# Performance work log

Hardware: AMD Instinct MI355X
Metric: run time of the kernel (lower is better)

Reference implementation:

```python
import jax, jax.numpy as jnp
import numpy as np

N = 100000
E = 3200000
D_IN = 256
D_HID = 256
D_OUT = 128
EPS = 1e-12


def setup_inputs() -> dict:
    key = jax.random.key(0)
    ks = jax.random.split(key, 8)
    x = jax.random.normal(ks[0], (N, D_IN), dtype=jnp.float32)
    edge_src = jax.random.randint(ks[1], (E,), 0, N, dtype=jnp.int32)
    edge_dst = jax.random.randint(ks[2], (E,), 0, N, dtype=jnp.int32)
    # mean aggregation: each row of the sparse adj sums to 1 -> val = 1/deg(src row)
    deg = jax.ops.segment_sum(jnp.ones((E,), jnp.float32), edge_src, num_segments=N)
    edge_val = 1.0 / jnp.maximum(deg, 1.0)[edge_src]
    # Xavier-uniform linear weights (torch Linear: y = x @ W.T + b); store as [in, out]
    def xavier(k, fan_in, fan_out):
        lim = jnp.sqrt(6.0 / (fan_in + fan_out))
        return jax.random.uniform(k, (fan_in, fan_out), jnp.float32, -lim, lim)
    W1 = xavier(ks[3], 2 * D_IN, D_HID)
    b1 = jnp.zeros((D_HID,), jnp.float32)
    W2 = xavier(ks[4], 2 * D_HID, D_OUT)
    b2 = jnp.zeros((D_OUT,), jnp.float32)
    return {"x": x, "edge_src": edge_src, "edge_dst": edge_dst, "edge_val": edge_val,
            "W1": W1, "b1": b1, "W2": W2, "b2": b2}


def _sage_layer(feat, edge_src, edge_dst, edge_val, W, b):
    # spmm: out[i] = sum_j adj[i,j] * feat[j]  (COO rows=edge_src, cols=edge_dst)
    msg = feat[edge_dst] * edge_val[:, None]              # [E, d]
    neigh = jax.ops.segment_sum(msg, edge_src, num_segments=feat.shape[0])  # [N, d]
    combined = jnp.concatenate([feat, neigh], axis=1) @ W + b  # [N, d_out]
    # F.normalize(p=2, dim=1): x / max(||x||_2, eps)
    norm = jnp.sqrt(jnp.sum(combined * combined, axis=1, keepdims=True))
    return combined / jnp.maximum(norm, EPS)


def reference(x, edge_src, edge_dst, edge_val, W1, b1, W2, b2):
    h = _sage_layer(x, edge_src, edge_dst, edge_val, W1, b1)
    h = jax.nn.relu(h)
    # dropout is identity at inference (training=False)
    return _sage_layer(h, edge_src, edge_dst, edge_val, W2, b2)
```

## Files before the change

### kernel.cpp

```cpp
#include <hip/hip_runtime.h>


#define N_NODES 100000
#define N_EDGES 3200000
#define DF      256
#define NRANGE  4

typedef __bf16 bf16x8 __attribute__((ext_vector_type(8)));
typedef float  f32x4  __attribute__((ext_vector_type(4)));
typedef float  f32x2  __attribute__((ext_vector_type(2)));

__device__ __forceinline__ ushort f2bf(float f){
  uint u = __float_as_uint(f);
  u += 0x7fffu + ((u >> 16) & 1u);
  return (ushort)(u >> 16);
}
__device__ __forceinline__ float bflo(uint u){ return __uint_as_float(u << 16); }
__device__ __forceinline__ float bfhi(uint u){ return __uint_as_float(u & 0xffff0000u); }


__global__ void k_cvt(const float4* __restrict__ x4, uint4* __restrict__ outb,
                      uint2* __restrict__ outq, int n8, int* __restrict__ deg, int nz){
  int i = blockIdx.x * blockDim.x + threadIdx.x;
  if(i < nz) deg[i] = 0;
  if(i >= n8) return;
  const float4 p = x4[2*i], q = x4[2*i+1];
  uint4 o;
  o.x = (uint)f2bf(p.x) | ((uint)f2bf(p.y) << 16);
  o.y = (uint)f2bf(p.z) | ((uint)f2bf(p.w) << 16);
  o.z = (uint)f2bf(q.x) | ((uint)f2bf(q.y) << 16);
  o.w = (uint)f2bf(q.z) | ((uint)f2bf(q.w) << 16);
  outb[i] = o;
  uint w0 = __builtin_amdgcn_cvt_pk_fp8_f32(p.x, p.y, 0u, false);
  w0      = __builtin_amdgcn_cvt_pk_fp8_f32(p.z, p.w, w0, true);
  uint w1 = __builtin_amdgcn_cvt_pk_fp8_f32(q.x, q.y, 0u, false);
  w1      = __builtin_amdgcn_cvt_pk_fp8_f32(q.z, q.w, w1, true);
  outq[i] = make_uint2(w0, w1);
}


__global__ void k_deg(const int* __restrict__ esrc, const float* __restrict__ eval,
                      int* __restrict__ deg, int E){
  int i = blockIdx.x * blockDim.x + threadIdx.x;
  if(i < E){
    const int   s = __builtin_nontemporal_load(&esrc[i]);
    const float v = __builtin_nontemporal_load(&eval[i]);
    deg[s] = (int)roundf(1.0f / v);
  }
}


__global__ void k_scan1(const int* __restrict__ deg, int* __restrict__ rowptr,
                        int* __restrict__ partials, int n){
  __shared__ int s[256];
  const int t = threadIdx.x;
  const int base = blockIdx.x * 1024 + t * 4;
  int v[4], run[4];
  #pragma unroll
  for(int j = 0; j < 4; j++) v[j] = (base + j < n) ? deg[base + j] : 0;
  int sum = 0;
  #pragma unroll
  for(int j = 0; j < 4; j++){ run[j] = sum; sum += v[j]; }
  s[t] = sum;
  __syncthreads();
  for(int off = 1; off < 256; off <<= 1){
    int x = (t >= off) ? s[t - off] : 0;
    __syncthreads();
    s[t] += x;
    __syncthreads();
  }
  const int texcl = s[t] - sum;
  #pragma unroll
  for(int j = 0; j < 4; j++) if(base + j < n) rowptr[base + j] = texcl + run[j];
  if(t == 255) partials[blockIdx.x] = s[255];
}

__global__ void k_scan2(int* __restrict__ partials, int nb,
                        int* __restrict__ rowptr, int n, int E){
  __shared__ int s[128];
  const int t = threadIdx.x;
  int v = (t < nb) ? partials[t] : 0;
  s[t] = v;
  __syncthreads();
  for(int off = 1; off < 128; off <<= 1){
    int x = (t >= off) ? s[t - off] : 0;
    __syncthreads();
    s[t] += x;
    __syncthreads();
  }
  if(t < nb) partials[t] = s[t] - v;
  if(t == 0) rowptr[n] = E;
}


__global__ void k_scan3(int* __restrict__ rowptr, const int* __restrict__ partials,
                        int* __restrict__ cursor, int n){
  int i = blockIdx.x * blockDim.x + threadIdx.x;
  if(i < n){
    const int v = rowptr[i] + partials[i >> 10];
    rowptr[i] = v;
    cursor[i] = v;
  }
}


__global__ void k_fill(const int* __restrict__ src, const int* __restrict__ dst,
                       int* __restrict__ cursor, int* __restrict__ col,
                       int E, int lo, int hi){
  int i = blockIdx.x * blockDim.x + threadIdx.x;
  if(i < E){
    const int r = src[i];
    if(r >= lo && r < hi){
      const int p = atomicAdd(&cursor[r], 1);
      col[p] = dst[i];
    }
  }
}


__device__ __forceinline__ void pack_frag(const float* __restrict__ W, uint4* __restrict__ Wp,
                                          int DOUT, int ksteps, int krow0, int tid){
  const int l   = tid & 63;
  const int s   = (tid >> 6) % ksteps;
  const int n   = tid / (64 * ksteps);
  const int grp = l >> 4, li = l & 15;
  const int col = n * 16 + li;
  ushort b[8];
  #pragma unroll
  for(int i = 0; i < 8; i++){
    const int k = krow0 + s * 32 + grp * 8 + i;
    b[i] = f2bf(W[(size_t)k * DOUT + col]);
  }
  uint4 o;
  o.x = (uint)b[0] | ((uint)b[1] << 16);
  o.y = (uint)b[2] | ((uint)b[3] << 16);
  o.z = (uint)b[4] | ((uint)b[5] << 16);
  o.w = (uint)b[6] | ((uint)b[7] << 16);
  Wp[tid] = o;
}

__global__ void k_packall(const float* __restrict__ W1, const float* __restrict__ W2,
                          uint4* __restrict__ Wp1, uint4* __restrict__ Wp2a,
                          uint4* __restrict__ Wp2b){
  const int tid = blockIdx.x * blockDim.x + threadIdx.x;
  if(tid < 16384)       pack_frag(W1, Wp1,  256, 16,   0, tid);
  else if(tid < 20480)  pack_frag(W2, Wp2a, 128,  8,   0, tid - 16384);
  else if(tid < 24576)  pack_frag(W2, Wp2b, 128,  8, 256, tid - 20480);
}


template<int RB>
__global__ __launch_bounds__(256)
void k_gather_q(const uchar* __restrict__ xq, const int* __restrict__ rowptr,
                const int* __restrict__ colidx, ushort* __restrict__ nbuf, int Nn){
  constexpr int LPR = RB / 16;
  constexpr int EPG = 64 / LPR;
  const int node = (blockIdx.x * blockDim.x + threadIdx.x) >> 6;
  const int lane = threadIdx.x & 63;
  if(node >= Nn) return;
  const int half = lane / LPR;
  const int li   = lane % LPR;
  const int s0 = rowptr[node];
  const int s1 = rowptr[node + 1];
  const float invd = (s1 > s0) ? (1.0f / (float)(s1 - s0)) : 0.0f;
  const uint cmax = (uint)(Nn - 1);
  float a[16];
  #pragma unroll
  for(int i = 0; i < 16; i++) a[i] = 0.f;

  #define DECODE_ACC(v)                                                        \
    {                                                                          \
      const uint uu[4] = {(v).x, (v).y, (v).z, (v).w};                         \
      _Pragma("unroll")                                                        \
      for(int m = 0; m < 4; m++){                                              \
        f32x2 lo = __builtin_amdgcn_cvt_pk_f32_fp8(uu[m], false);              \
        f32x2 hi = __builtin_amdgcn_cvt_pk_f32_fp8(uu[m], true);               \
        a[m*4+0] += lo.x; a[m*4+1] += lo.y;                                    \
        a[m*4+2] += hi.x; a[m*4+3] += hi.y;                                    \
      }                                                                        \
    }

  int e = s0;
  for(; e + 4 * EPG <= s1; e += 4 * EPG){
    uint c[4];
    #pragma unroll
    for(int j = 0; j < 4; j++)
      c[j] = min((uint)__builtin_nontemporal_load(&colidx[e + j * EPG + half]), cmax);
    uint4 v[4];
    #pragma unroll
    for(int j = 0; j < 4; j++) v[j] = *(const uint4*)(xq + (size_t)c[j] * RB + li * 16);
    #pragma unroll
    for(int j = 0; j < 4; j++) DECODE_ACC(v[j]);
  }
  for(; e + EPG <= s1; e += EPG){
    const uint c = min((uint)__builtin_nontemporal_load(&colidx[e + half]), cmax);
    const uint4 v = *(const uint4*)(xq + (size_t)c * RB + li * 16);
    DECODE_ACC(v);
  }
  if(half < s1 - e){
    const uint c = min((uint)__builtin_nontemporal_load(&colidx[e + half]), cmax);
    const uint4 v = *(const uint4*)(xq + (size_t)c * RB + li * 16);
    DECODE_ACC(v);
  }
  #undef DECODE_ACC

  #pragma unroll
  for(int off = LPR; off < 64; off <<= 1)
    #pragma unroll
    for(int i = 0; i < 16; i++) a[i] += __shfl_xor(a[i], off);

  if(lane < LPR){
    uint4 o1, o2;
    o1.x = (uint)f2bf(a[ 0]*invd) | ((uint)f2bf(a[ 1]*invd) << 16);
    o1.y = (uint)f2bf(a[ 2]*invd) | ((uint)f2bf(a[ 3]*invd) << 16);
    o1.z = (uint)f2bf(a[ 4]*invd) | ((uint)f2bf(a[ 5]*invd) << 16);
    o1.w = (uint)f2bf(a[ 6]*invd) | ((uint)f2bf(a[ 7]*invd) << 16);
    o2.x = (uint)f2bf(a[ 8]*invd) | ((uint)f2bf(a[ 9]*invd) << 16);
    o2.y = (uint)f2bf(a[10]*invd) | ((uint)f2bf(a[11]*invd) << 16);
    o2.z = (uint)f2bf(a[12]*invd) | ((uint)f2bf(a[13]*invd) << 16);
    o2.w = (uint)f2bf(a[14]*invd) | ((uint)f2bf(a[15]*invd) << 16);
    ushort* p = nbuf + (size_t)node * RB + li * 16;
    *(uint4*)(p)     = o1;
    *(uint4*)(p + 8) = o2;
  }
}


template<int DOUT, int KS, bool TWOSRC, bool ADDG, bool RELU, bool NORM, int OMODE>
__launch_bounds__(256, 2)
__global__ void k_mlp(const ushort* __restrict__ A0, const ushort* __restrict__ A1,
                      const uint4* __restrict__ Wp, const float* __restrict__ bias,
                      const ushort* __restrict__ g,
                      void* __restrict__ outp, int Nn)
{
  constexpr int NT   = DOUT / 16;
  constexpr int DIMA = TWOSRC ? KS * 16 : KS * 32;
  const int l     = threadIdx.x & 63;
  const int w     = threadIdx.x >> 6;
  const int nodeb = blockIdx.x * 64 + w * 16;
  const int grp   = l >> 4;
  const int li    = l & 15;

  const int rowL = min(nodeb + li, Nn - 1);
  uint4 a[KS];
  if(TWOSRC){
    const ushort* xr = A0 + (size_t)rowL * DIMA;
    const ushort* nr = A1 + (size_t)rowL * DIMA;
    #pragma unroll
    for(int s = 0; s < KS/2; s++) a[s]        = *(const uint4*)(xr + s * 32 + grp * 8);
    #pragma unroll
    for(int s = 0; s < KS/2; s++) a[s + KS/2] = *(const uint4*)(nr + s * 32 + grp * 8);
  } else {
    const ushort* xr = A0 + (size_t)rowL * DIMA;
    #pragma unroll
    for(int s = 0; s < KS; s++) a[s] = *(const uint4*)(xr + s * 32 + grp * 8);
  }

  f32x4 acc[NT];
  #pragma unroll
  for(int n = 0; n < NT; n++){
    f32x4 c = {0.f, 0.f, 0.f, 0.f};
    #pragma unroll
    for(int s = 0; s < KS; s++){
      const uint4 b = Wp[(size_t)(n * KS + s) * 64 + l];
      c = __builtin_amdgcn_mfma_f32_16x16x32_bf16(
            __builtin_bit_cast(bf16x8, a[s]),
            __builtin_bit_cast(bf16x8, b), c, 0, 0, 0);
    }
    acc[n] = c;
  }

  if(NORM){
    #pragma unroll
    for(int n = 0; n < NT; n++){
      const float bv = bias[n * 16 + li];
      acc[n][0] += bv; acc[n][1] += bv; acc[n][2] += bv; acc[n][3] += bv;
    }
  }

  if(ADDG){
    #pragma unroll
    for(int r = 0; r < 4; r++){
      const int rowg = min(nodeb + grp * 4 + r, Nn - 1);
      const uint4 gv = *(const uint4*)(g + (size_t)rowg * DOUT + li * 8);
      acc[0][r] += bflo(gv.x); acc[1][r] += bfhi(gv.x);
      acc[2][r] += bflo(gv.y); acc[3][r] += bfhi(gv.y);
      acc[4][r] += bflo(gv.z); acc[5][r] += bfhi(gv.z);
      acc[6][r] += bflo(gv.w); acc[7][r] += bfhi(gv.w);
    }
  }

  float rn[4] = {1.f, 1.f, 1.f, 1.f};
  if(NORM){
    #pragma unroll
    for(int r = 0; r < 4; r++){
      float ss = 0.f;
      #pragma unroll
      for(int n = 0; n < NT; n++) ss = fmaf(acc[n][r], acc[n][r], ss);
      ss += __shfl_xor(ss, 1);
      ss += __shfl_xor(ss, 2);
      ss += __shfl_xor(ss, 4);
      ss += __shfl_xor(ss, 8);
      rn[r] = 1.0f / fmaxf(sqrtf(ss), 1e-12f);
    }
  }

  #pragma unroll
  for(int r = 0; r < 4; r++){
    const int node = nodeb + grp * 4 + r;
    if(node < Nn){
      if(OMODE == 2){
        uint w0 = __builtin_amdgcn_cvt_pk_fp8_f32(acc[0][r], acc[1][r], 0u, false);
        w0      = __builtin_amdgcn_cvt_pk_fp8_f32(acc[2][r], acc[3][r], w0, true);
        uint w1 = __builtin_amdgcn_cvt_pk_fp8_f32(acc[4][r], acc[5][r], 0u, false);
        w1      = __builtin_amdgcn_cvt_pk_fp8_f32(acc[6][r], acc[7][r], w1, true);
        *(uint2*)((uchar*)outp + (size_t)node * DOUT + li * 8) = make_uint2(w0, w1);
      } else {
        #pragma unroll
        for(int n = 0; n < NT; n++){
          float y = acc[n][r];
          if(NORM) y *= rn[r];
          if(RELU) y = fmaxf(y, 0.0f);
          const size_t idx = (size_t)node * DOUT + n * 16 + li;
          if(OMODE == 1) ((ushort*)outp)[idx] = f2bf(y);
          else           ((float*)outp)[idx]  = y;
        }
      }
    }
  }
}


extern "C" void kernel_launch(void* const* d_in, const int* in_sizes, int n_in,
                              void* d_out, int out_size, void* d_ws, size_t ws_size,
                              hipStream_t stream) {
  const float* x    = (const float*)d_in[0];
  const int*   esrc = (const int*)  d_in[1];
  const int*   edst = (const int*)  d_in[2];
  const float* eval = (const float*)d_in[3];
  const float* W1   = (const float*)d_in[4];
  const float* b1   = (const float*)d_in[5];
  const float* W2   = (const float*)d_in[6];
  const float* b2   = (const float*)d_in[7];
  float* out = (float*)d_out;

  const int N = N_NODES, E = N_EDGES;

  char* ws = (char*)d_ws;
  size_t off = 0;
  auto alloc = [&](size_t bytes) -> void* {
    void* p = ws + off;
    off += (bytes + 255) & ~(size_t)255;
    return p;
  };
  int*    deg      = (int*)   alloc((size_t)N * 4);
  int*    rowptr   = (int*)   alloc((size_t)(N + 1) * 4);
  int*    cursor   = (int*)   alloc((size_t)N * 4);
  int*    partials = (int*)   alloc(512);
  int*    colidx   = (int*)   alloc((size_t)E * 4);
  ushort* xbuf     = (ushort*)alloc((size_t)N * DF * 2);
  uchar*  xq       = (uchar*) alloc((size_t)N * DF);
  ushort* hbuf     = (ushort*)alloc((size_t)N * DF * 2);
  ushort* nbuf     = (ushort*)alloc((size_t)N * DF * 2);
  uint4*  Wp1      = (uint4*) alloc((size_t)16 * 16 * 64 * 16);
  uint4*  Wp2a     = (uint4*) alloc((size_t) 8 *  8 * 64 * 16);
  uint4*  Wp2b     = (uint4*) alloc((size_t) 8 *  8 * 64 * 16);
  if(off > ws_size) return;

  uchar*  Pq = (uchar*)nbuf;
  ushort* gb = nbuf + (size_t)N * 64;

  const int NBLK_SCAN = (N + 1023) / 1024;
  const int n8 = N * DF / 8;

  k_cvt  <<<(n8 + 255) / 256, 256, 0, stream>>>((const float4*)x, (uint4*)xbuf,
                                                (uint2*)xq, n8, deg, N);
  k_deg  <<<(E + 255) / 256, 256, 0, stream>>>(esrc, eval, deg, E);
  k_packall<<<96, 256, 0, stream>>>(W1, W2, Wp1, Wp2a, Wp2b);

  k_scan1<<<NBLK_SCAN,       256, 0, stream>>>(deg, rowptr, partials, N);
  k_scan2<<<1,               128, 0, stream>>>(partials, NBLK_SCAN, rowptr, N, E);
  k_scan3<<<(N + 255) / 256, 256, 0, stream>>>(rowptr, partials, cursor, N);
  const int RSPAN = N / NRANGE;
  for(int r = 0; r < NRANGE; r++)
    k_fill<<<(E + 255) / 256, 256, 0, stream>>>(esrc, edst, cursor, colidx,
                                                E, r * RSPAN, (r + 1) * RSPAN);

  const int GRID_MLP = (N + 63) / 64;

  k_gather_q<256><<<N / 4, 256, 0, stream>>>(xq, rowptr, colidx, nbuf, N);
  k_mlp<256, 16, true, false, true, true, 1>
      <<<GRID_MLP, 256, 0, stream>>>(xbuf, nbuf, Wp1, b1, nullptr, hbuf, N);

  k_mlp<128, 8, false, false, false, false, 2>
      <<<GRID_MLP, 256, 0, stream>>>(hbuf, nullptr, Wp2b, nullptr, nullptr, Pq, N);
  k_gather_q<128><<<N / 4, 256, 0, stream>>>(Pq, rowptr, colidx, gb, N);
  k_mlp<128, 8, false, true, false, true, 0>
      <<<GRID_MLP, 256, 0, stream>>>(hbuf, nullptr, Wp2a, b2, gb, out, N);
}
```

Baseline: 604.5 us.

## Fuse layer-1 MLP with layer-2 neighbor projection via LDS-staged hidden tile

Adds a fused kernel that computes the layer-1 linear, bias, L2-normalize and ReLU, then stages each wave's 16-row hidden tile in shared memory and immediately multiplies it by the layer-2 neighbor weights, writing FP8 projections. This removes a separate kernel launch and the re-read of hbuf from global memory for the projection. Pq gets its own buffer instead of aliasing nbuf. The gather accumulator also switches to packed float2 adds to cut VALU instructions. The cost is higher register and LDS pressure in the fused kernel, which may reduce occupancy.

```diff
diff --git a/kernel.cpp b/kernel.cpp
--- a/kernel.cpp
+++ b/kernel.cpp
@@ -92,7 +92,6 @@
   if(t == 0) rowptr[n] = E;
 }
 
-
 __global__ void k_scan3(int* __restrict__ rowptr, const int* __restrict__ partials,
                         int* __restrict__ cursor, int n){
   int i = blockIdx.x * blockDim.x + threadIdx.x;
@@ -164,9 +163,9 @@
   const int s1 = rowptr[node + 1];
   const float invd = (s1 > s0) ? (1.0f / (float)(s1 - s0)) : 0.0f;
   const uint cmax = (uint)(Nn - 1);
-  float a[16];
-  #pragma unroll
-  for(int i = 0; i < 16; i++) a[i] = 0.f;
+  f32x2 a2[8];
+  #pragma unroll
+  for(int i = 0; i < 8; i++) a2[i] = (f32x2){0.f, 0.f};
 
   #define DECODE_ACC(v)                                                        \
     {                                                                          \
@@ -175,8 +174,8 @@
       for(int m = 0; m < 4; m++){                                              \
         f32x2 lo = __builtin_amdgcn_cvt_pk_f32_fp8(uu[m], false);              \
         f32x2 hi = __builtin_amdgcn_cvt_pk_f32_fp8(uu[m], true);               \
-        a[m*4+0] += lo.x; a[m*4+1] += lo.y;                                    \
-        a[m*4+2] += hi.x; a[m*4+3] += hi.y;                                    \
+        a2[2*m]   += lo;                                                       \
+        a2[2*m+1] += hi;                                                       \
       }                                                                        \
     }
 
@@ -203,6 +202,10 @@
     DECODE_ACC(v);
   }
   #undef DECODE_ACC
+
+  float a[16];
+  #pragma unroll
+  for(int i = 0; i < 8; i++){ a[2*i] = a2[i].x; a[2*i+1] = a2[i].y; }
 
   #pragma unroll
   for(int off = LPR; off < 64; off <<= 1)
@@ -222,6 +225,101 @@
     ushort* p = nbuf + (size_t)node * RB + li * 16;
     *(uint4*)(p)     = o1;
     *(uint4*)(p + 8) = o2;
+  }
+}
+
+
+__launch_bounds__(256, 2)
+__global__ void k_mlp1p(const ushort* __restrict__ xb, const ushort* __restrict__ nb,
+                        const uint4* __restrict__ Wp1, const float* __restrict__ b1,
+                        const uint4* __restrict__ Wp2b,
+                        ushort* __restrict__ hbuf, uchar* __restrict__ Pq, int Nn)
+{
+  __shared__ ushort hT[4][16][264];
+  const int l     = threadIdx.x & 63;
+  const int w     = threadIdx.x >> 6;
+  const int nodeb = blockIdx.x * 64 + w * 16;
+  const int grp   = l >> 4;
+  const int li    = l & 15;
+
+  const int rowL = min(nodeb + li, Nn - 1);
+  const ushort* xr = xb + (size_t)rowL * DF;
+  const ushort* nr = nb + (size_t)rowL * DF;
+  uint4 a[16];
+  #pragma unroll
+  for(int s = 0; s < 8; s++) a[s]     = *(const uint4*)(xr + s * 32 + grp * 8);
+  #pragma unroll
+  for(int s = 0; s < 8; s++) a[s + 8] = *(const uint4*)(nr + s * 32 + grp * 8);
+
+  f32x4 acc[16];
+  #pragma unroll
+  for(int n = 0; n < 16; n++){
+    f32x4 c = {0.f, 0.f, 0.f, 0.f};
+    #pragma unroll
+    for(int s = 0; s < 16; s++){
+      const uint4 b = Wp1[(size_t)(n * 16 + s) * 64 + l];
+      c = __builtin_amdgcn_mfma_f32_16x16x32_bf16(
+            __builtin_bit_cast(bf16x8, a[s]),
+            __builtin_bit_cast(bf16x8, b), c, 0, 0, 0);
+    }
+    acc[n] = c;
+  }
+
+  #pragma unroll
+  for(int n = 0; n < 16; n++){
+    const float bv = b1[n * 16 + li];
+    acc[n][0] += bv; acc[n][1] += bv; acc[n][2] += bv; acc[n][3] += bv;
+  }
+
+  #pragma unroll
+  for(int r = 0; r < 4; r++){
+    float ss = 0.f;
+    #pragma unroll
+    for(int n = 0; n < 16; n++) ss = fmaf(acc[n][r], acc[n][r], ss);
+    ss += __shfl_xor(ss, 1);
+    ss += __shfl_xor(ss, 2);
+    ss += __shfl_xor(ss, 4);
+    ss += __shfl_xor(ss, 8);
+    const float rn = 1.0f / fmaxf(sqrtf(ss), 1e-12f);
+    const int row  = grp * 4 + r;
+    const int node = nodeb + row;
+    #pragma unroll
+    for(int n = 0; n < 16; n++){
+      const ushort hv = f2bf(fmaxf(acc[n][r] * rn, 0.0f));
+      hT[w][row][n * 16 + li] = hv;
+      if(node < Nn) hbuf[(size_t)node * DF + n * 16 + li] = hv;
+    }
+  }
+  __syncthreads();
+
+  uint4 pa[8];
+  #pragma unroll
+  for(int s = 0; s < 8; s++) pa[s] = *(const uint4*)&hT[w][li][s * 32 + grp * 8];
+
+  f32x4 pacc[8];
+  #pragma unroll
+  for(int n = 0; n < 8; n++){
+    f32x4 c = {0.f, 0.f, 0.f, 0.f};
+    #pragma unroll
+    for(int s = 0; s < 8; s++){
+      const uint4 b = Wp2b[(size_t)(n * 8 + s) * 64 + l];
+      c = __builtin_amdgcn_mfma_f32_16x16x32_bf16(
+            __builtin_bit_cast(bf16x8, pa[s]),
+            __builtin_bit_cast(bf16x8, b), c, 0, 0, 0);
+    }
+    pacc[n] = c;
+  }
+
+  #pragma unroll
+  for(int r = 0; r < 4; r++){
+    const int node = nodeb + grp * 4 + r;
+    if(node < Nn){
+      uint w0 = __builtin_amdgcn_cvt_pk_fp8_f32(pacc[0][r], pacc[1][r], 0u, false);
+      w0      = __builtin_amdgcn_cvt_pk_fp8_f32(pacc[2][r], pacc[3][r], w0, true);
+      uint w1 = __builtin_amdgcn_cvt_pk_fp8_f32(pacc[4][r], pacc[5][r], 0u, false);
+      w1      = __builtin_amdgcn_cvt_pk_fp8_f32(pacc[6][r], pacc[7][r], w1, true);
+      *(uint2*)(Pq + (size_t)node * 128 + li * 8) = make_uint2(w0, w1);
+    }
   }
 }
 
@@ -362,13 +460,13 @@
   uchar*  xq       = (uchar*) alloc((size_t)N * DF);
   ushort* hbuf     = (ushort*)alloc((size_t)N * DF * 2);
   ushort* nbuf     = (ushort*)alloc((size_t)N * DF * 2);
+  uchar*  Pq       = (uchar*) alloc((size_t)N * 128);
   uint4*  Wp1      = (uint4*) alloc((size_t)16 * 16 * 64 * 16);
   uint4*  Wp2a     = (uint4*) alloc((size_t) 8 *  8 * 64 * 16);
   uint4*  Wp2b     = (uint4*) alloc((size_t) 8 *  8 * 64 * 16);
   if(off > ws_size) return;
 
-  uchar*  Pq = (uchar*)nbuf;
-  ushort* gb = nbuf + (size_t)N * 64;
+  ushort* gb = nbuf;
 
   const int NBLK_SCAN = (N + 1023) / 1024;
   const int n8 = N * DF / 8;
@@ -389,11 +487,8 @@
   const int GRID_MLP = (N + 63) / 64;
 
   k_gather_q<256><<<N / 4, 256, 0, stream>>>(xq, rowptr, colidx, nbuf, N);
-  k_mlp<256, 16, true, false, true, true, 1>
-      <<<GRID_MLP, 256, 0, stream>>>(xbuf, nbuf, Wp1, b1, nullptr, hbuf, N);
-
-  k_mlp<128, 8, false, false, false, false, 2>
-      <<<GRID_MLP, 256, 0, stream>>>(hbuf, nullptr, Wp2b, nullptr, nullptr, Pq, N);
+  k_mlp1p<<<GRID_MLP, 256, 0, stream>>>(xbuf, nbuf, Wp1, b1, Wp2b, hbuf, Pq, N);
+
   k_gather_q<128><<<N / 4, 256, 0, stream>>>(Pq, rowptr, colidx, gb, N);
   k_mlp<128, 8, false, true, false, true, 0>
       <<<GRID_MLP, 256, 0, stream>>>(hbuf, nullptr, Wp2a, b2, gb, out, N);
```

Measured after the change: 580.9 us. 1.04x faster.
